# Kernel optimization log

Measured on AMD Instinct MI355X. Metric: run time of the kernel, lower is better.

## Reference

```python
import jax, jax.numpy as jnp
import numpy as np

N0, N1, N2 = 1500, 6000, 4000
F_IN, F_OUT = 32, 32
K00, K0P = 2, 2
K1N, K11, K12, K1P = 2, 2, 2, 2
K2N, K22 = 2, 2


def chebyshev(L, k, x):
    # Chebyshev recursion: T1 = L x, T2 = 2 L T1 - x, T_j = 2 L T_{j-1} - T_{j-2}
    # Returns (n, F, k) stack of T1..Tk (identity term handled by caller).
    t_prev = L @ x
    terms = [t_prev]
    t_pp = x
    for _ in range(k - 1):
        t = 2.0 * (L @ t_prev) - t_pp
        t_pp, t_prev = t_prev, t
        terms.append(t)
    return jnp.stack(terms, axis=2)


def _sym(key, n):
    a = jax.random.normal(key, (n, n), jnp.float32) / jnp.sqrt(jnp.float32(n))
    return 0.5 * (a + a.T)


def setup_inputs():
    key = jax.random.key(0)
    ks = jax.random.split(key, 16)
    x0 = jax.random.normal(ks[0], (N0, F_IN), jnp.float32)
    x1 = jax.random.normal(ks[1], (N1, F_IN), jnp.float32)
    x2 = jax.random.normal(ks[2], (N2, F_IN), jnp.float32)
    B1 = jax.random.normal(ks[3], (N0, N1), jnp.float32) / jnp.sqrt(jnp.float32(N1))
    B2 = jax.random.normal(ks[4], (N1, N2), jnp.float32) / jnp.sqrt(jnp.float32(N2))
    L0 = _sym(ks[5], N0)
    L1l = _sym(ks[6], N1)
    L1u = _sym(ks[7], N1)
    L2 = _sym(ks[8], N2)
    # Degree matrices: diagonal with strictly positive entries (as in real SC data).
    D1 = jnp.diag(jax.random.uniform(ks[9], (N0,), jnp.float32, 0.5, 2.0))
    D2 = jnp.diag(jax.random.uniform(ks[10], (N1,), jnp.float32, 0.5, 2.0))
    D3 = jnp.diag(jax.random.uniform(ks[11], (N2,), jnp.float32, 0.5, 2.0))
    D5 = jnp.diag(jax.random.uniform(ks[12], (N1,), jnp.float32, 0.5, 2.0))
    W0 = jax.random.normal(ks[13], (F_IN, F_OUT, 1 + K00 + 1 + K0P), jnp.float32) * 0.05
    W1 = jax.random.normal(ks[14], (F_IN, F_OUT, 1 + K1N + 1 + K11 + K12 + 1 + K1P), jnp.float32) * 0.05
    W2 = jax.random.normal(ks[15], (F_IN, F_OUT, 1 + K2N + 1 + K22), jnp.float32) * 0.05
    return dict(x0=x0, x1=x1, x2=x2, B1=B1, B2=B2, L0=L0, L1l=L1l, L1u=L1u,
                L2=L2, D1=D1, D2=D2, D3=D3, D5=D5, W0=W0, W1=W1, W2=W2)


def _forward(x0, x1, x2, B1, B2, L0, L1l, L1u, L2, d1_inv, d2, d3, d5_pinv, W0, W1, W2):
    # ---- order 0 ----
    x0p = d1_inv[:, None] * (B1 @ x1)               # inv(D1) @ B1 @ x1
    X0 = jnp.concatenate([x0[:, :, None], chebyshev(L0, K00, x0),
                          x0p[:, :, None], chebyshev(L0, K0P, x0p)], axis=2)
    # ---- order 1 ----
    x1n = d2[:, None] * (B1.T @ (d1_inv[:, None] * x0))  # D2 @ B1.T @ inv(D1) @ x0
    x1p = B2 @ (d3[:, None] * x2)                        # B2 @ D3 @ x2
    X1 = jnp.concatenate([x1n[:, :, None], chebyshev(L1l, K1N, x1n),
                          x1[:, :, None], chebyshev(L1l, K11, x1), chebyshev(L1u, K12, x1),
                          x1p[:, :, None], chebyshev(L1u, K1P, x1p)], axis=2)
    # ---- order 2 ----
    x2n = B2.T @ (d5_pinv[:, None] * x1)                 # B2.T @ pinv(D5) @ x1
    X2 = jnp.concatenate([x2n[:, :, None], chebyshev(L2, K2N, x2n),
                          x2[:, :, None], chebyshev(L2, K22, x2)], axis=2)
    y0 = jax.nn.relu(jnp.einsum('nik,iok->no', X0, W0))
    y1 = jax.nn.relu(jnp.einsum('nik,iok->no', X1, W1))
    y2 = jax.nn.relu(jnp.einsum('nik,iok->no', X2, W2))
    return (y0, y1, y2)


def reference(x0, x1, x2, B1, B2, L0, L1l, L1u, L2, D1, D2, D3, D5, W0, W1, W2):
    # D matrices are diagonal degree matrices; inverse/pinverse of a diagonal
    # matrix is the diagonal of (safe) reciprocals -- identical math to
    # torch.inverse / torch.pinverse on these inputs, without an O(n^3) solve.
    d1_inv = 1.0 / jnp.diag(D1)
    d2 = jnp.diag(D2)
    d3 = jnp.diag(D3)
    d5 = jnp.diag(D5)
    d5_pinv = jnp.where(d5 != 0, 1.0 / d5, 0.0)
    return _forward(x0, x1, x2, B1, B2, L0, L1l, L1u, L2, d1_inv, d2, d3, d5_pinv, W0, W1, W2)
```

## Files before the change

### kernel.cpp

```cpp
#include <hip/hip_runtime.h>
#include <stdint.h>

typedef __attribute__((ext_vector_type(4))) float f32x4;
typedef __attribute__((ext_vector_type(8))) short s16x8;
typedef unsigned short us;

static __device__ __forceinline__ us f2bf(float f) {
  union { float f; uint32_t u; } v; v.f = f;
  uint32_t u = v.u;
  u += 0x7fffu + ((u >> 16) & 1u);
  return (us)(u >> 16);
}

static __device__ __forceinline__ float dval(const float* dv, long r, long dstr, int mode) {
  if (!dv || mode == 0) return 1.f;
  float d = dv[r * dstr];
  if (mode == 2) return (d != 0.f) ? 1.f / d : 0.f;
  return d;
}

static __device__ void tpose_tile(const float* __restrict__ src, long lds_, int n,
                                  const float* __restrict__ dv, long dstr, int mode,
                                  us* __restrict__ dst, int ldn, int tile,
                                  us (*sm)[72]) {
  const int t = threadIdx.x;
  const int r0 = tile * 64;
  {
    const int rr = t & 63;
    const int cg = t >> 6;
    const int gr = r0 + rr;
    float sc = 1.f;
    f32x4 v0 = {0.f, 0.f, 0.f, 0.f}, v1 = {0.f, 0.f, 0.f, 0.f};
    if (gr < n) {
      sc = dval(dv, gr, dstr, mode);
      const float* sp = src + (long)gr * lds_ + cg * 8;
      v0 = *(const f32x4*)sp;
      v1 = *(const f32x4*)(sp + 4);
    }
#pragma unroll
    for (int j = 0; j < 4; ++j) {
      sm[cg * 8 + j][rr] = f2bf(v0[j] * sc);
      sm[cg * 8 + 4 + j][rr] = f2bf(v1[j] * sc);
    }
  }
  __syncthreads();
  {
    const int f = t >> 3;
    const int nc = (t & 7) * 8;
    if (r0 + nc < ldn) {
      s16x8 v = *(const s16x8*)&sm[f][nc];
      *(s16x8*)(dst + (size_t)f * ldn + r0 + nc) = v;
    }
  }
}

static __device__ void convT_tile(const float* __restrict__ in, int ldi, int nI, int nC,
                                  us* __restrict__ outT, int ldoT, int bx, int by,
                                  us (*sT)[72]) {
  const int t = threadIdx.x;
  const int tc0 = bx * 64;
  const int tr0 = by * 64;
  const int c0 = (t & 15) * 4;
  const int r0 = (t >> 4) * 4;
  us ub[4][4];
#pragma unroll
  for (int j = 0; j < 4; ++j) {
    int gr = tr0 + r0 + j;
    f32x4 v = {0.f, 0.f, 0.f, 0.f};
    if (gr < nI) {
      const float* pI = in + (size_t)gr * ldi + tc0 + c0;
      if (tc0 + c0 + 3 < nC) {
        v = *(const f32x4*)pI;
      } else {
#pragma unroll
        for (int jj = 0; jj < 4; ++jj) if (tc0 + c0 + jj < nC) v[jj] = pI[jj];
      }
    }
#pragma unroll
    for (int jj = 0; jj < 4; ++jj) ub[j][jj] = f2bf(v[jj]);
  }
#pragma unroll
  for (int jj = 0; jj < 4; ++jj) {
    union { us u[4]; unsigned long long ll; } w;
#pragma unroll
    for (int j = 0; j < 4; ++j) w.u[j] = ub[j][jj];
    *(unsigned long long*)&sT[c0 + jj][r0] = w.ll;
  }
  __syncthreads();
#pragma unroll
  for (int p = 0; p < 2; ++p) {
    int orow = (t >> 3) + p * 32;
    int rcol = (t & 7) * 8;
    int grow = tc0 + orow;
    int gcol = tr0 + rcol;
    if (grow < nC && gcol < ldoT) {
      union { unsigned long long ll[2]; s16x8 v; } w;
      w.ll[0] = *(const unsigned long long*)&sT[orow][rcol];
      w.ll[1] = *(const unsigned long long*)&sT[orow][rcol + 4];
      *(s16x8*)(outT + (size_t)grow * ldoT + gcol) = w.v;
    }
  }
}

struct TSeg { const float* src; us* dst; int lds_, n, ldn, start; };
struct TPack { TSeg t[8]; int nseg; };

__global__ __launch_bounds__(256) void tpose_batch(TPack P) {
  __shared__ us sm[32][72];
  int b = blockIdx.x;
  int si = P.nseg - 1;
  while (si > 0 && P.t[si].start > b) --si;
  const TSeg s = P.t[si];
  tpose_tile(s.src, s.lds_, s.n, nullptr, 0, 0, s.dst, s.ldn, b - s.start, sm);
}

__global__ __launch_bounds__(256) void prep(
    const float* __restrict__ x0, const float* __restrict__ x1, const float* __restrict__ x2,
    const float* __restrict__ D1, const float* __restrict__ D3, const float* __restrict__ D5,
    const float* __restrict__ W0, const float* __restrict__ W1, const float* __restrict__ W2,
    us* x0T, us* x0dT, us* x1T, us* x1dT, us* x2T, us* x2dT,
    us* W0T, us* W1T, us* W2T,
    float* __restrict__ X0a, float* __restrict__ X1a, float* __restrict__ X2a) {
  __shared__ us sm[32][72];
  int b = blockIdx.x;
  if (b < 24)  { tpose_tile(x0, 32, 1500, nullptr, 0, 0, x0T, 1536, b, sm); return; }
  b -= 24;
  if (b < 24)  { tpose_tile(x0, 32, 1500, D1, 1501, 2, x0dT, 1536, b, sm); return; }
  b -= 24;
  if (b < 94)  { tpose_tile(x1, 32, 6000, nullptr, 0, 0, x1T, 6016, b, sm); return; }
  b -= 94;
  if (b < 94)  { tpose_tile(x1, 32, 6000, D5, 6001, 2, x1dT, 6016, b, sm); return; }
  b -= 94;
  if (b < 63)  { tpose_tile(x2, 32, 4000, nullptr, 0, 0, x2T, 4032, b, sm); return; }
  b -= 63;
  if (b < 63)  { tpose_tile(x2, 32, 4000, D3, 4001, 1, x2dT, 4032, b, sm); return; }
  b -= 63;
  if (b < 3) {
    const float* W = (b == 0) ? W0 : ((b == 1) ? W1 : W2);
    us* dst = (b == 0) ? W0T : ((b == 1) ? W1T : W2T);
    const int K = (b == 1) ? 11 : 6;
    const int C = K * 32;
    const int CP = (b == 1) ? 384 : 192;
    for (int idx = threadIdx.x; idx < 32 * CP; idx += 256) {
      int o = idx / CP, j = idx - o * CP;
      float v = 0.f;
      if (j < C) { int k = j >> 5, i = j & 31; v = W[((long)i * 32 + o) * K + k]; }
      dst[(size_t)o * CP + j] = f2bf(v);
    }
    return;
  }
  b -= 3;
  const long V0 = 1500L * 48, V1 = 6000L * 88, V2 = 4000L * 48;
  for (long i = (long)b * 256 + threadIdx.x; i < V0 + V1 + V2; i += 512L * 256) {
    f32x4 v = {0.f, 0.f, 0.f, 0.f};
    float* dst;
    if (i < V0) {
      long r = i / 48; int c0 = (int)(i - r * 48) * 4;
      if (c0 < 32) v = *(const f32x4*)(x0 + r * 32 + c0);
      dst = X0a + r * 192 + c0;
    } else if (i < V0 + V1) {
      long j = i - V0; long r = j / 88; int c0 = (int)(j - r * 88) * 4;
      if (c0 >= 96 && c0 < 128) v = *(const f32x4*)(x1 + r * 32 + (c0 - 96));
      dst = X1a + r * 352 + c0;
    } else {
      long j = i - V0 - V1; long r = j / 48; int c0 = (int)(j - r * 48) * 4;
      if (c0 >= 96 && c0 < 128) v = *(const f32x4*)(x2 + r * 32 + (c0 - 96));
      dst = X2a + r * 192 + c0;
    }
    *(f32x4*)dst = v;
  }
}

struct Seg {
  const void* A;
  const us* Bt0; const us* Bt1;
  const float* S0; const float* S1; const float* sv;
  float* C0; float* C1;
  float alpha, beta;
  int lda, ldS, sstr, ldc;
  int n_rows, n_k, ldb, smode, kchunk, tiles, ky, start;
};
struct CSeg { const float* in; us* out; int ldi, nI, nC, ldoT, cx, start; };
struct Mega {
  Seg s[4]; CSeg c[2]; TSeg t[2];
  int nseg, gemm_end, nconv, conv_end, ntp;
};

template <int F, bool RELU, typename AT>
__global__ __launch_bounds__(256) void mega(Mega P) {
  __shared__ __align__(16) us lds[64 * 128];
  const int b = blockIdx.x;
  if (b >= P.gemm_end) {
    if (b < P.conv_end) {
      int lb = b - P.gemm_end;
      int si = P.nconv - 1;
      while (si > 0 && P.c[si].start > lb) --si;
      const CSeg s = P.c[si];
      int l = lb - s.start;
      convT_tile(s.in, s.ldi, s.nI, s.nC, s.out, s.ldoT, l % s.cx, l / s.cx, (us(*)[72])lds);
    } else {
      int lb = b - P.conv_end;
      int si = P.ntp - 1;
      while (si > 0 && P.t[si].start > lb) --si;
      const TSeg s = P.t[si];
      tpose_tile(s.src, s.lds_, s.n, nullptr, 0, 0, s.dst, s.ldn, lb - s.start, (us(*)[72])lds);
    }
    return;
  }

  us* sA = lds;
  us* sX = lds + 64 * 64;

  int si = P.nseg - 1;
  while (si > 0 && P.s[si].start > b) --si;
  const Seg sg = P.s[si];
  const int local = b - sg.start;
  const int bx = local % sg.tiles;
  const int kidx = local / sg.tiles;

  const AT* __restrict__ A = (const AT*)sg.A;
  const int n_rows = sg.n_rows, n_k = sg.n_k, ldb = sg.ldb;

  const int tid = threadIdx.x;
  const int k_begin = kidx * sg.kchunk;
  const int k_end = min(n_k, k_begin + sg.kchunk);
  const int nsteps = (k_end - k_begin + 63) >> 6;

  const int srow = tid >> 2;
  const int sslot = tid & 3;
  const int kc_off = sslot * 16;
  const long arowg = (long)bx * 64 + srow;
  const bool arow_ok = arowg < n_rows;
  const bool xrow_ok = (F == 64) || (srow < 32);
  const us* xbase = ((srow < 32) ? sg.Bt0 : sg.Bt1) + (size_t)(srow & 31) * ldb;

  s16x8 abf0 = (s16x8)0, abf1 = (s16x8)0;
  f32x4 af0, af1, af2, af3;
  s16x8 x0r = (s16x8)0, x1r = (s16x8)0;

  auto load_tiles = [&](int k0) {
    int kc = k0 + kc_off;
    if constexpr (sizeof(AT) == 4) {
      af0 = f32x4{0, 0, 0, 0}; af1 = af0; af2 = af0; af3 = af0;
      if (arow_ok) {
        const float* ap = (const float*)A + (size_t)arowg * sg.lda + kc;
        if (kc + 15 < n_k) {
          af0 = *(const f32x4*)ap; af1 = *(const f32x4*)(ap + 4);
          af2 = *(const f32x4*)(ap + 8); af3 = *(const f32x4*)(ap + 12);
        } else {
#pragma unroll
          for (int j = 0; j < 4; ++j) {
            if (kc + j < n_k) af0[j] = ap[j];
            if (kc + 4 + j < n_k) af1[j] = ap[4 + j];
            if (kc + 8 + j < n_k) af2[j] = ap[8 + j];
            if (kc + 12 + j < n_k) af3[j] = ap[12 + j];
          }
        }
      }
    } else {
      abf0 = (s16x8)0; abf1 = (s16x8)0;
      if (arow_ok) {
        const us* ap = (const us*)A + (size_t)arowg * sg.lda + kc;
        if (kc + 15 < n_k) {
          abf0 = *(const s16x8*)ap; abf1 = *(const s16x8*)(ap + 8);
        } else {
#pragma unroll
          for (int j = 0; j < 8; ++j) {
            if (kc + j < n_k) abf0[j] = (short)ap[j];
            if (kc + 8 + j < n_k) abf1[j] = (short)ap[8 + j];
          }
        }
      }
    }
    if (xrow_ok) {
      x0r = *(const s16x8*)(xbase + kc);
      x1r = *(const s16x8*)(xbase + kc + 8);
    }
  };

  load_tiles(k_begin);

  const int wave = tid >> 6;
  const int lane = tid & 63;
  const int g = lane >> 4;
  const int r = lane & 15;
  const int wslot0 = ((2 * sslot) ^ (srow & 7)) * 8;
  const int wslot1 = ((2 * sslot + 1) ^ (srow & 7)) * 8;

  f32x4 acc[F / 16];
#pragma unroll
  for (int i = 0; i < F / 16; ++i) acc[i] = f32x4{0.f, 0.f, 0.f, 0.f};

  for (int s = 0; s < nsteps; ++s) {
    s16x8 pk0, pk1;
    if constexpr (sizeof(AT) == 4) {
#pragma unroll
      for (int j = 0; j < 4; ++j) {
        pk0[j] = (short)f2bf(af0[j]); pk0[4 + j] = (short)f2bf(af1[j]);
        pk1[j] = (short)f2bf(af2[j]); pk1[4 + j] = (short)f2bf(af3[j]);
      }
    } else { pk0 = abf0; pk1 = abf1; }
    *(s16x8*)&sA[srow * 64 + wslot0] = pk0;
    *(s16x8*)&sA[srow * 64 + wslot1] = pk1;
    if (xrow_ok) {
      *(s16x8*)&sX[srow * 64 + wslot0] = x0r;
      *(s16x8*)&sX[srow * 64 + wslot1] = x1r;
    }
    __syncthreads();
    if (s + 1 < nsteps) load_tiles(k_begin + (s + 1) * 64);

    const int arow = wave * 16 + r;
#pragma unroll
    for (int kk = 0; kk < 2; ++kk) {
      s16x8 afr = *(s16x8*)&sA[arow * 64 + (((kk * 4 + g) ^ (arow & 7)) << 3)];
#pragma unroll
      for (int nt = 0; nt < F / 16; ++nt) {
        int xc = nt * 16 + r;
        s16x8 bfr = *(s16x8*)&sX[xc * 64 + (((kk * 4 + g) ^ (xc & 7)) << 3)];
        acc[nt] = __builtin_amdgcn_mfma_f32_16x16x32_bf16(afr, bfr, acc[nt], 0, 0, 0);
      }
    }
    __syncthreads();
  }

  float svv[4];
#pragma unroll
  for (int j = 0; j < 4; ++j) {
    long row = (long)bx * 64 + wave * 16 + g * 4 + j;
    svv[j] = (row < n_rows) ? dval(sg.sv, row, sg.sstr, sg.smode) : 0.f;
  }
#pragma unroll
  for (int nt = 0; nt < F / 16; ++nt) {
    float* C = (F == 64 && nt >= 2) ? sg.C1 : sg.C0;
    const float* S = (F == 64 && nt >= 2) ? sg.S1 : sg.S0;
    int col = ((F == 64) ? (nt & 1) : nt) * 16 + r;
#pragma unroll
    for (int j = 0; j < 4; ++j) {
      long row = (long)bx * 64 + wave * 16 + g * 4 + j;
      if (row < n_rows) {
        float v = sg.alpha * acc[nt][j] * svv[j];
        if (S && (sg.ky == 1 || kidx == 0)) v += sg.beta * S[row * (size_t)sg.ldS + col];
        if (sg.ky > 1) {
          atomicAdd(&C[row * (size_t)sg.ldc + col], v);
        } else {
          if (RELU) v = fmaxf(v, 0.0f);
          C[row * (size_t)sg.ldc + col] = v;
        }
      }
    }
  }
}

__global__ void colcopy(float* __restrict__ dst, const float* __restrict__ src, int n,
                        const float* __restrict__ dv, long dstr, int mode) {
  int idx = blockIdx.x * 256 + threadIdx.x;
  if (idx >= n * 32) return;
  dst[idx] = src[idx] * dval(dv, idx >> 5, dstr, mode);
}
__global__ void scale_ld(float* __restrict__ dst, long ld, int n,
                         const float* __restrict__ dv, long dstr, int mode) {
  int idx = blockIdx.x * 256 + threadIdx.x;
  if (idx >= n * 32) return;
  dst[(size_t)(idx >> 5) * ld + (idx & 31)] *= dval(dv, idx >> 5, dstr, mode);
}
__global__ __launch_bounds__(256) void mm_at(
    const float* __restrict__ A, int lda, int m,
    const float* __restrict__ X,
    float* __restrict__ C, int ldc, int n, int kchunk) {
  const int fg = threadIdx.x & 3;
  const int cg = threadIdx.x >> 2;
  const int c = blockIdx.x * 256 + cg * 4;
  const int k0 = blockIdx.y * kchunk;
  const int k1 = min(m, k0 + kchunk);
  const int f = fg * 8;
  float acc[4][8];
#pragma unroll
  for (int a = 0; a < 4; ++a)
#pragma unroll
    for (int bb = 0; bb < 8; ++bb) acc[a][bb] = 0.f;
  for (int k = k0; k < k1; ++k) {
    const float* Ar = A + (size_t)k * lda + c;
    f32x4 a;
    if (c + 3 < n) a = *(const f32x4*)Ar;
    else {
      a = f32x4{0.f, 0.f, 0.f, 0.f};
#pragma unroll
      for (int j = 0; j < 4; ++j) if (c + j < n) a[j] = Ar[j];
    }
    f32x4 xa = *(const f32x4*)(X + (size_t)k * 32 + f);
    f32x4 xb = *(const f32x4*)(X + (size_t)k * 32 + f + 4);
#pragma unroll
    for (int cc = 0; cc < 4; ++cc)
#pragma unroll
      for (int jj = 0; jj < 4; ++jj) {
        acc[cc][jj] += a[cc] * xa[jj];
        acc[cc][4 + jj] += a[cc] * xb[jj];
      }
  }
  if (c >= n) return;
#pragma unroll
  for (int cc = 0; cc < 4; ++cc) {
    if (c + cc >= n) break;
#pragma unroll
    for (int jj = 0; jj < 8; ++jj)
      atomicAdd(&C[(size_t)(c + cc) * ldc + f + jj], acc[cc][jj]);
  }
}


extern "C" void kernel_launch(void* const* d_in, const int* in_sizes, int n_in,
                              void* d_out, int out_size, void* d_ws, size_t ws_size,
                              hipStream_t stream) {
  (void)in_sizes; (void)n_in; (void)out_size;
  const float* x0  = (const float*)d_in[0];
  const float* x1  = (const float*)d_in[1];
  const float* x2  = (const float*)d_in[2];
  const float* B1  = (const float*)d_in[3];
  const float* B2  = (const float*)d_in[4];
  const float* L0  = (const float*)d_in[5];
  const float* L1l = (const float*)d_in[6];
  const float* L1u = (const float*)d_in[7];
  const float* L2  = (const float*)d_in[8];
  const float* D1  = (const float*)d_in[9];
  const float* D2  = (const float*)d_in[10];
  const float* D3  = (const float*)d_in[11];
  const float* D5  = (const float*)d_in[12];
  const float* W0  = (const float*)d_in[13];
  const float* W1  = (const float*)d_in[14];
  const float* W2  = (const float*)d_in[15];
  float* out = (float*)d_out;

  char* p = (char*)d_ws;
  auto alloc = [&](size_t b) { char* r = p; p += (b + 255) & ~(size_t)255; return r; };

  us* x0T   = (us*)alloc((size_t)32 * 1536 * 2);
  us* x0dT  = (us*)alloc((size_t)32 * 1536 * 2);
  us* x1T   = (us*)alloc((size_t)32 * 6016 * 2);
  us* x1dT  = (us*)alloc((size_t)32 * 6016 * 2);
  us* x2T   = (us*)alloc((size_t)32 * 4032 * 2);
  us* x2dT  = (us*)alloc((size_t)32 * 4032 * 2);
  us* x0pT  = (us*)alloc((size_t)32 * 1536 * 2);
  us* x1nT  = (us*)alloc((size_t)32 * 6016 * 2);
  us* x1pT  = (us*)alloc((size_t)32 * 6016 * 2);
  us* x2nT  = (us*)alloc((size_t)32 * 4032 * 2);
  us* T1a0T = (us*)alloc((size_t)32 * 1536 * 2);
  us* T1b0T = (us*)alloc((size_t)32 * 1536 * 2);
  us* T1laT = (us*)alloc((size_t)32 * 6016 * 2);
  us* T1lbT = (us*)alloc((size_t)32 * 6016 * 2);
  us* T1uaT = (us*)alloc((size_t)32 * 6016 * 2);
  us* T1ubT = (us*)alloc((size_t)32 * 6016 * 2);
  us* T1a2T = (us*)alloc((size_t)32 * 4032 * 2);
  us* T1b2T = (us*)alloc((size_t)32 * 4032 * 2);
  us* W0T   = (us*)alloc((size_t)32 * 192 * 2);
  us* W1T   = (us*)alloc((size_t)32 * 384 * 2);
  us* W2T   = (us*)alloc((size_t)32 * 192 * 2);

  float* X0a = (float*)alloc((size_t)1500 * 192 * 4);
  float* X1a = (float*)alloc((size_t)6000 * 352 * 4);
  float* X2a = (float*)alloc((size_t)4000 * 192 * 4);

  float* z0  = (float*)alloc((size_t)1500 * 32 * 4);
  float* sx1 = (float*)alloc((size_t)6000 * 32 * 4);

  size_t used = (size_t)(p - (char*)d_ws);
  const size_t needB = (size_t)6000 * 1536 * 2 + (size_t)4000 * 6016 * 2 + 1024;
  bool haveB = used + needB <= ws_size;
  us *B1t = nullptr, *B2t = nullptr;
  if (haveB) {
    B1t = (us*)alloc((size_t)6000 * 1536 * 2);
    B2t = (us*)alloc((size_t)4000 * 6016 * 2);
  }

  auto nb = [](long t) { return (unsigned)((t + 255) / 256); };
  auto seg = [](const void* A, int lda, int n_rows, int n_k,
                const us* Bt0, const us* Bt1, int ldb,
                float alpha, const float* S0, const float* S1, int ldS, float beta,
                const float* sv, int sstr, int smode,
                float* C0, float* C1, int ldc,
                int kchunk, int tiles, int ky, int start) {
    Seg s;
    s.A = A; s.Bt0 = Bt0; s.Bt1 = Bt1; s.S0 = S0; s.S1 = S1; s.sv = sv;
    s.C0 = C0; s.C1 = C1; s.alpha = alpha; s.beta = beta;
    s.lda = lda; s.ldS = ldS; s.sstr = sstr; s.ldc = ldc;
    s.n_rows = n_rows; s.n_k = n_k; s.ldb = ldb; s.smode = smode;
    s.kchunk = kchunk; s.tiles = tiles; s.ky = ky; s.start = start;
    return s;
  };

  prep<<<877, 256, 0, stream>>>(x0, x1, x2, D1, D3, D5, W0, W1, W2,
                                x0T, x0dT, x1T, x1dT, x2T, x2dT, W0T, W1T, W2T,
                                X0a, X1a, X2a);

  {
    Mega P{};
    P.nseg = 2;
    P.s[0] = seg(B1, 6000, 1500, 6000, x1T, x1T, 6016,
                 1.f, nullptr, nullptr, 0, 0.f, D1, 1501, 2,
                 X0a + 3 * 32, nullptr, 192, 768, 24, 8, 0);
    P.s[1] = seg(B2, 4000, 6000, 4000, x2dT, x2dT, 4032,
                 1.f, nullptr, nullptr, 0, 0.f, nullptr, 0, 0,
                 X1a + 8 * 32, nullptr, 352, 512, 94, 8, 192);
    P.gemm_end = 944;
    if (haveB) {
      P.nconv = 2;
      P.c[0] = CSeg{B1, B1t, 6000, 1500, 6000, 1536, 94, 0};
      P.c[1] = CSeg{B2, B2t, 4000, 6000, 4000, 6016, 63, 2256};
      P.conv_end = 944 + 8178;
    } else {
      P.nconv = 0; P.conv_end = 944;
    }
    P.ntp = 0;
    mega<32, false, float><<<P.conv_end, 256, 0, stream>>>(P);
  }

  if (haveB) {
    Mega P{};
    P.nseg = 2;
    P.s[0] = seg(B1t, 1536, 6000, 1536, x0dT, x0dT, 1536,
                 1.f, nullptr, nullptr, 0, 0.f, D2, 6001, 1,
                 X1a + 0 * 32, nullptr, 352, 384, 94, 4, 0);
    P.s[1] = seg(B2t, 6016, 4000, 6016, x1dT, x1dT, 6016,
                 1.f, nullptr, nullptr, 0, 0.f, nullptr, 0, 0,
                 X2a + 0 * 32, nullptr, 192, 768, 63, 8, 376);
    P.gemm_end = 880;
    P.nconv = 0; P.conv_end = 880;
    P.ntp = 2;
    P.t[0] = TSeg{X0a + 3 * 32, x0pT, 192, 1500, 1536, 0};
    P.t[1] = TSeg{X1a + 8 * 32, x1pT, 352, 6000, 6016, 24};
    mega<32, false, us><<<998, 256, 0, stream>>>(P);
  } else {
    colcopy<<<nb(1500L * 32), 256, 0, stream>>>(z0, x0, 1500, D1, 1501, 2);
    mm_at<<<dim3(24, 24), 256, 0, stream>>>(B1, 6000, 1500, z0, X1a + 0 * 32, 352, 6000, 63);
    scale_ld<<<nb(6000L * 32), 256, 0, stream>>>(X1a + 0 * 32, 352, 6000, D2, 6001, 1);
    colcopy<<<nb(6000L * 32), 256, 0, stream>>>(sx1, x1, 6000, D5, 6001, 2);
    mm_at<<<dim3(16, 32), 256, 0, stream>>>(B2, 4000, 6000, sx1, X2a + 0 * 32, 192, 4000, 188);
    TPack T{};
    T.nseg = 2;
    T.t[0] = TSeg{X0a + 3 * 32, x0pT, 192, 1500, 1536, 0};
    T.t[1] = TSeg{X1a + 8 * 32, x1pT, 352, 6000, 6016, 24};
    tpose_batch<<<118, 256, 0, stream>>>(T);
  }

  {
    TPack T{};
    T.nseg = 2;
    T.t[0] = TSeg{X1a + 0 * 32, x1nT, 352, 6000, 6016, 0};
    T.t[1] = TSeg{X2a + 0 * 32, x2nT, 192, 4000, 4032, 94};
    tpose_batch<<<157, 256, 0, stream>>>(T);
  }

  {
    Mega P{};
    P.nseg = 4;
    P.s[0] = seg(L0, 1500, 1500, 1500, x0T, x0pT, 1536,
                 1.f, nullptr, nullptr, 0, 0.f, nullptr, 0, 0,
                 X0a + 1 * 32, X0a + 4 * 32, 192, 768, 24, 2, 0);
    P.s[1] = seg(L1l, 6000, 6000, 6000, x1nT, x1T, 6016,
                 1.f, nullptr, nullptr, 0, 0.f, nullptr, 0, 0,
                 X1a + 1 * 32, X1a + 4 * 32, 352, 1536, 94, 4, 48);
    P.s[2] = seg(L1u, 6000, 6000, 6000, x1T, x1pT, 6016,
                 1.f, nullptr, nullptr, 0, 0.f, nullptr, 0, 0,
                 X1a + 6 * 32, X1a + 9 * 32, 352, 1536, 94, 4, 424);
    P.s[3] = seg(L2, 4000, 4000, 4000, x2nT, x2T, 4032,
                 1.f, nullptr, nullptr, 0, 0.f, nullptr, 0, 0,
                 X2a + 1 * 32, X2a + 4 * 32, 192, 1024, 63, 4, 800);
    P.gemm_end = 1052; P.nconv = 0; P.conv_end = 1052; P.ntp = 0;
    mega<64, false, float><<<1052, 256, 0, stream>>>(P);
  }

  {
    TPack T{};
    T.nseg = 8;
    T.t[0] = TSeg{X0a + 1 * 32, T1a0T, 192, 1500, 1536, 0};
    T.t[1] = TSeg{X0a + 4 * 32, T1b0T, 192, 1500, 1536, 24};
    T.t[2] = TSeg{X1a + 1 * 32, T1laT, 352, 6000, 6016, 48};
    T.t[3] = TSeg{X1a + 4 * 32, T1lbT, 352, 6000, 6016, 142};
    T.t[4] = TSeg{X1a + 6 * 32, T1uaT, 352, 6000, 6016, 236};
    T.t[5] = TSeg{X1a + 9 * 32, T1ubT, 352, 6000, 6016, 330};
    T.t[6] = TSeg{X2a + 1 * 32, T1a2T, 192, 4000, 4032, 424};
    T.t[7] = TSeg{X2a + 4 * 32, T1b2T, 192, 4000, 4032, 487};
    tpose_batch<<<550, 256, 0, stream>>>(T);
  }

  {
    Mega P{};
    P.nseg = 4;
    P.s[0] = seg(L0, 1500, 1500, 1500, T1a0T, T1b0T, 1536,
                 2.f, X0a + 0 * 32, X0a + 3 * 32, 192, -1.f, nullptr, 0, 0,
                 X0a + 2 * 32, X0a + 5 * 32, 192, 768, 24, 2, 0);
    P.s[1] = seg(L1l, 6000, 6000, 6000, T1laT, T1lbT, 6016,
                 2.f, X1a + 0 * 32, X1a + 3 * 32, 352, -1.f, nullptr, 0, 0,
                 X1a + 2 * 32, X1a + 5 * 32, 352, 1536, 94, 4, 48);
    P.s[2] = seg(L1u, 6000, 6000, 6000, T1uaT, T1ubT, 6016,
                 2.f, X1a + 3 * 32, X1a + 8 * 32, 352, -1.f, nullptr, 0, 0,
                 X1a + 7 * 32, X1a + 10 * 32, 352, 1536, 94, 4, 424);
    P.s[3] = seg(L2, 4000, 4000, 4000, T1a2T, T1b2T, 4032,
                 2.f, X2a + 0 * 32, X2a + 3 * 32, 192, -1.f, nullptr, 0, 0,
                 X2a + 2 * 32, X2a + 5 * 32, 192, 1024, 63, 4, 800);
    P.gemm_end = 1052; P.nconv = 0; P.conv_end = 1052; P.ntp = 0;
    mega<64, false, float><<<1052, 256, 0, stream>>>(P);
  }

  {
    Mega P{};
    P.nseg = 3;
    P.s[0] = seg(X0a, 192, 1500, 192, W0T, W0T, 192,
                 1.f, nullptr, nullptr, 0, 0.f, nullptr, 0, 0,
                 out, nullptr, 32, 192, 24, 1, 0);
    P.s[1] = seg(X1a, 352, 6000, 352, W1T, W1T, 384,
                 1.f, nullptr, nullptr, 0, 0.f, nullptr, 0, 0,
                 out + 48000, nullptr, 32, 384, 94, 1, 24);
    P.s[2] = seg(X2a, 192, 4000, 192, W2T, W2T, 192,
                 1.f, nullptr, nullptr, 0, 0.f, nullptr, 0, 0,
                 out + 240000, nullptr, 32, 192, 63, 1, 118);
    P.gemm_end = 181; P.nconv = 0; P.conv_end = 181; P.ntp = 0;
    mega<32, true, float><<<181, 256, 0, stream>>>(P);
  }
}
```

Measured before the change: 308.0 us.

## Double-buffer LDS tiles and prefetch two K-steps ahead in GEMM loop

Splits the shared-memory staging into two ping-pong buffers and keeps two register sets of prefetched global tiles, so loads run two K-steps ahead. This drops the trailing __syncthreads per step, leaving one barrier per step, and replaces the leading one with an explicit lgkmcnt wait plus s_barrier fenced by sched_barriers. It raises LDS use to 32 KB and the register pressure, which can lower occupancy.

```diff
diff --git a/kernel.cpp b/kernel.cpp
--- a/kernel.cpp
+++ b/kernel.cpp
@@ -188,7 +188,7 @@
 
 template <int F, bool RELU, typename AT>
 __global__ __launch_bounds__(256) void mega(Mega P) {
-  __shared__ __align__(16) us lds[64 * 128];
+  __shared__ __align__(16) us lds[4 * 64 * 64];
   const int b = blockIdx.x;
   if (b >= P.gemm_end) {
     if (b < P.conv_end) {
@@ -208,9 +208,6 @@
     return;
   }
 
-  us* sA = lds;
-  us* sX = lds + 64 * 64;
-
   int si = P.nseg - 1;
   while (si > 0 && P.s[si].start > b) --si;
   const Seg sg = P.s[si];
@@ -234,51 +231,50 @@
   const bool xrow_ok = (F == 64) || (srow < 32);
   const us* xbase = ((srow < 32) ? sg.Bt0 : sg.Bt1) + (size_t)(srow & 31) * ldb;
 
-  s16x8 abf0 = (s16x8)0, abf1 = (s16x8)0;
-  f32x4 af0, af1, af2, af3;
-  s16x8 x0r = (s16x8)0, x1r = (s16x8)0;
-
-  auto load_tiles = [&](int k0) {
+  f32x4 aA0, aA1, aA2, aA3, aB0, aB1, aB2, aB3;
+  s16x8 bA0 = (s16x8)0, bA1 = (s16x8)0, bB0 = (s16x8)0, bB1 = (s16x8)0;
+  s16x8 xA0 = (s16x8)0, xA1 = (s16x8)0, xB0 = (s16x8)0, xB1 = (s16x8)0;
+
+  auto load_set = [&](int k0, f32x4& a0, f32x4& a1, f32x4& a2, f32x4& a3,
+                      s16x8& b0, s16x8& b1, s16x8& xx0, s16x8& xx1) {
     int kc = k0 + kc_off;
     if constexpr (sizeof(AT) == 4) {
-      af0 = f32x4{0, 0, 0, 0}; af1 = af0; af2 = af0; af3 = af0;
+      a0 = f32x4{0, 0, 0, 0}; a1 = a0; a2 = a0; a3 = a0;
       if (arow_ok) {
         const float* ap = (const float*)A + (size_t)arowg * sg.lda + kc;
         if (kc + 15 < n_k) {
-          af0 = *(const f32x4*)ap; af1 = *(const f32x4*)(ap + 4);
-          af2 = *(const f32x4*)(ap + 8); af3 = *(const f32x4*)(ap + 12);
+          a0 = *(const f32x4*)ap; a1 = *(const f32x4*)(ap + 4);
+          a2 = *(const f32x4*)(ap + 8); a3 = *(const f32x4*)(ap + 12);
         } else {
 #pragma unroll
           for (int j = 0; j < 4; ++j) {
-            if (kc + j < n_k) af0[j] = ap[j];
-            if (kc + 4 + j < n_k) af1[j] = ap[4 + j];
-            if (kc + 8 + j < n_k) af2[j] = ap[8 + j];
-            if (kc + 12 + j < n_k) af3[j] = ap[12 + j];
+            if (kc + j < n_k) a0[j] = ap[j];
+            if (kc + 4 + j < n_k) a1[j] = ap[4 + j];
+            if (kc + 8 + j < n_k) a2[j] = ap[8 + j];
+            if (kc + 12 + j < n_k) a3[j] = ap[12 + j];
           }
         }
       }
     } else {
-      abf0 = (s16x8)0; abf1 = (s16x8)0;
+      b0 = (s16x8)0; b1 = (s16x8)0;
       if (arow_ok) {
         const us* ap = (const us*)A + (size_t)arowg * sg.lda + kc;
         if (kc + 15 < n_k) {
-          abf0 = *(const s16x8*)ap; abf1 = *(const s16x8*)(ap + 8);
+          b0 = *(const s16x8*)ap; b1 = *(const s16x8*)(ap + 8);
         } else {
 #pragma unroll
           for (int j = 0; j < 8; ++j) {
-            if (kc + j < n_k) abf0[j] = (short)ap[j];
-            if (kc + 8 + j < n_k) abf1[j] = (short)ap[8 + j];
+            if (kc + j < n_k) b0[j] = (short)ap[j];
+            if (kc + 8 + j < n_k) b1[j] = (short)ap[8 + j];
           }
         }
       }
     }
     if (xrow_ok) {
-      x0r = *(const s16x8*)(xbase + kc);
-      x1r = *(const s16x8*)(xbase + kc + 8);
+      xx0 = *(const s16x8*)(xbase + kc);
+      xx1 = *(const s16x8*)(xbase + kc + 8);
     }
   };
-
-  load_tiles(k_begin);
 
   const int wave = tid >> 6;
   const int lane = tid & 63;
@@ -291,24 +287,29 @@
 #pragma unroll
   for (int i = 0; i < F / 16; ++i) acc[i] = f32x4{0.f, 0.f, 0.f, 0.f};
 
-  for (int s = 0; s < nsteps; ++s) {
+  auto step = [&](int s, int bufsel, f32x4& a0, f32x4& a1, f32x4& a2, f32x4& a3,
+                  s16x8& b0, s16x8& b1, s16x8& xx0, s16x8& xx1) {
+    us* sA = lds + (bufsel ? 8192 : 0);
+    us* sX = sA + 4096;
     s16x8 pk0, pk1;
     if constexpr (sizeof(AT) == 4) {
 #pragma unroll
       for (int j = 0; j < 4; ++j) {
-        pk0[j] = (short)f2bf(af0[j]); pk0[4 + j] = (short)f2bf(af1[j]);
-        pk1[j] = (short)f2bf(af2[j]); pk1[4 + j] = (short)f2bf(af3[j]);
+        pk0[j] = (short)f2bf(a0[j]); pk0[4 + j] = (short)f2bf(a1[j]);
+        pk1[j] = (short)f2bf(a2[j]); pk1[4 + j] = (short)f2bf(a3[j]);
       }
-    } else { pk0 = abf0; pk1 = abf1; }
+    } else { pk0 = b0; pk1 = b1; }
     *(s16x8*)&sA[srow * 64 + wslot0] = pk0;
     *(s16x8*)&sA[srow * 64 + wslot1] = pk1;
     if (xrow_ok) {
-      *(s16x8*)&sX[srow * 64 + wslot0] = x0r;
-      *(s16x8*)&sX[srow * 64 + wslot1] = x1r;
-    }
-    __syncthreads();
-    if (s + 1 < nsteps) load_tiles(k_begin + (s + 1) * 64);
-
+      *(s16x8*)&sX[srow * 64 + wslot0] = xx0;
+      *(s16x8*)&sX[srow * 64 + wslot1] = xx1;
+    }
+    __builtin_amdgcn_sched_barrier(0);
+    asm volatile("s_waitcnt lgkmcnt(0)" ::: "memory");
+    __builtin_amdgcn_s_barrier();
+    __builtin_amdgcn_sched_barrier(0);
+    if (s + 2 < nsteps) load_set(k_begin + (s + 2) * 64, a0, a1, a2, a3, b0, b1, xx0, xx1);
     const int arow = wave * 16 + r;
 #pragma unroll
     for (int kk = 0; kk < 2; ++kk) {
@@ -320,7 +321,13 @@
         acc[nt] = __builtin_amdgcn_mfma_f32_16x16x32_bf16(afr, bfr, acc[nt], 0, 0, 0);
       }
     }
-    __syncthreads();
+  };
+
+  load_set(k_begin, aA0, aA1, aA2, aA3, bA0, bA1, xA0, xA1);
+  if (nsteps > 1) load_set(k_begin + 64, aB0, aB1, aB2, aB3, bB0, bB1, xB0, xB1);
+  for (int s = 0; s < nsteps; s += 2) {
+    step(s, 0, aA0, aA1, aA2, aA3, bA0, bA1, xA0, xA1);
+    if (s + 1 < nsteps) step(s + 1, 1, aB0, aB1, aB2, aB3, bB0, bB1, xB0, xB1);
   }
 
   float svv[4];
```

New measurement: 313.4 us. About the same (+1.8%).

## Double GEMM row tile to 128 rows per block and rebalance K-splits

Applied to the files above, without the earlier changes.

The mega GEMM kernel now computes 128 rows per block: each wave handles two 16-row subtiles that share the same X fragments loaded from LDS, and each thread loads 32 A elements per step. Launch configurations are updated to halve the tile counts, and for the L1/L2 Chebyshev GEMMs the K-split is raised to keep the grid size similar. This is meant to reuse the staged X tile across twice as many A rows, cutting X global and LDS traffic. The cost is more LDS and registers per block, which can lower occupancy, and fewer blocks for the small GEMMs such as the final weight projection.

```diff
diff --git a/kernel.cpp b/kernel.cpp
--- a/kernel.cpp
+++ b/kernel.cpp
@@ -188,7 +188,7 @@
 
 template <int F, bool RELU, typename AT>
 __global__ __launch_bounds__(256) void mega(Mega P) {
-  __shared__ __align__(16) us lds[64 * 128];
+  __shared__ __align__(16) us lds[128 * 64 + 64 * 64];
   const int b = blockIdx.x;
   if (b >= P.gemm_end) {
     if (b < P.conv_end) {
@@ -209,7 +209,7 @@
   }
 
   us* sA = lds;
-  us* sX = lds + 64 * 64;
+  us* sX = lds + 128 * 64;
 
   int si = P.nseg - 1;
   while (si > 0 && P.s[si].start > b) --si;
@@ -226,55 +226,59 @@
   const int k_end = min(n_k, k_begin + sg.kchunk);
   const int nsteps = (k_end - k_begin + 63) >> 6;
 
-  const int srow = tid >> 2;
-  const int sslot = tid & 3;
-  const int kc_off = sslot * 16;
-  const long arowg = (long)bx * 64 + srow;
+  const int srowA = tid >> 1;
+  const int sslotA = tid & 1;
+  const int kcA = sslotA * 32;
+  const long arowg = (long)bx * 128 + srowA;
   const bool arow_ok = arowg < n_rows;
-  const bool xrow_ok = (F == 64) || (srow < 32);
-  const us* xbase = ((srow < 32) ? sg.Bt0 : sg.Bt1) + (size_t)(srow & 31) * ldb;
-
-  s16x8 abf0 = (s16x8)0, abf1 = (s16x8)0;
-  f32x4 af0, af1, af2, af3;
+  const int srowX = tid >> 2;
+  const int sslotX = tid & 3;
+  const int kcX = sslotX * 16;
+  const bool xrow_ok = (F == 64) || (srowX < 32);
+  const us* xbase = ((srowX < 32) ? sg.Bt0 : sg.Bt1) + (size_t)(srowX & 31) * ldb;
+
+  f32x4 af[8];
+  s16x8 abf[4];
   s16x8 x0r = (s16x8)0, x1r = (s16x8)0;
 
   auto load_tiles = [&](int k0) {
-    int kc = k0 + kc_off;
+    int kc = k0 + kcA;
     if constexpr (sizeof(AT) == 4) {
-      af0 = f32x4{0, 0, 0, 0}; af1 = af0; af2 = af0; af3 = af0;
+#pragma unroll
+      for (int h = 0; h < 8; ++h) af[h] = f32x4{0.f, 0.f, 0.f, 0.f};
       if (arow_ok) {
         const float* ap = (const float*)A + (size_t)arowg * sg.lda + kc;
-        if (kc + 15 < n_k) {
-          af0 = *(const f32x4*)ap; af1 = *(const f32x4*)(ap + 4);
-          af2 = *(const f32x4*)(ap + 8); af3 = *(const f32x4*)(ap + 12);
+        if (kc + 31 < n_k) {
+#pragma unroll
+          for (int h = 0; h < 8; ++h) af[h] = *(const f32x4*)(ap + 4 * h);
         } else {
 #pragma unroll
-          for (int j = 0; j < 4; ++j) {
-            if (kc + j < n_k) af0[j] = ap[j];
-            if (kc + 4 + j < n_k) af1[j] = ap[4 + j];
-            if (kc + 8 + j < n_k) af2[j] = ap[8 + j];
-            if (kc + 12 + j < n_k) af3[j] = ap[12 + j];
-          }
+          for (int h = 0; h < 8; ++h)
+#pragma unroll
+            for (int j = 0; j < 4; ++j)
+              if (kc + 4 * h + j < n_k) af[h][j] = ap[4 * h + j];
         }
       }
     } else {
-      abf0 = (s16x8)0; abf1 = (s16x8)0;
+#pragma unroll
+      for (int h = 0; h < 4; ++h) abf[h] = (s16x8)0;
       if (arow_ok) {
         const us* ap = (const us*)A + (size_t)arowg * sg.lda + kc;
-        if (kc + 15 < n_k) {
-          abf0 = *(const s16x8*)ap; abf1 = *(const s16x8*)(ap + 8);
+        if (kc + 31 < n_k) {
+#pragma unroll
+          for (int h = 0; h < 4; ++h) abf[h] = *(const s16x8*)(ap + 8 * h);
         } else {
 #pragma unroll
-          for (int j = 0; j < 8; ++j) {
-            if (kc + j < n_k) abf0[j] = (short)ap[j];
-            if (kc + 8 + j < n_k) abf1[j] = (short)ap[8 + j];
-          }
+          for (int h = 0; h < 4; ++h)
+#pragma unroll
+            for (int j = 0; j < 8; ++j)
+              if (kc + 8 * h + j < n_k) abf[h][j] = (short)ap[8 * h + j];
         }
       }
     }
     if (xrow_ok) {
-      x0r = *(const s16x8*)(xbase + kc);
-      x1r = *(const s16x8*)(xbase + kc + 8);
+      x0r = *(const s16x8*)(xbase + k0 + kcX);
+      x1r = *(const s16x8*)(xbase + k0 + kcX + 8);
     }
   };
 
@@ -284,67 +288,80 @@
   const int lane = tid & 63;
   const int g = lane >> 4;
   const int r = lane & 15;
-  const int wslot0 = ((2 * sslot) ^ (srow & 7)) * 8;
-  const int wslot1 = ((2 * sslot + 1) ^ (srow & 7)) * 8;
-
-  f32x4 acc[F / 16];
-#pragma unroll
-  for (int i = 0; i < F / 16; ++i) acc[i] = f32x4{0.f, 0.f, 0.f, 0.f};
+  const int wsX0 = ((2 * sslotX) ^ (srowX & 7)) * 8;
+  const int wsX1 = ((2 * sslotX + 1) ^ (srowX & 7)) * 8;
+
+  f32x4 acc[2][F / 16];
+#pragma unroll
+  for (int st = 0; st < 2; ++st)
+#pragma unroll
+    for (int i = 0; i < F / 16; ++i) acc[st][i] = f32x4{0.f, 0.f, 0.f, 0.f};
 
   for (int s = 0; s < nsteps; ++s) {
-    s16x8 pk0, pk1;
-    if constexpr (sizeof(AT) == 4) {
-#pragma unroll
-      for (int j = 0; j < 4; ++j) {
-        pk0[j] = (short)f2bf(af0[j]); pk0[4 + j] = (short)f2bf(af1[j]);
-        pk1[j] = (short)f2bf(af2[j]); pk1[4 + j] = (short)f2bf(af3[j]);
+#pragma unroll
+    for (int h = 0; h < 4; ++h) {
+      s16x8 pk;
+      if constexpr (sizeof(AT) == 4) {
+#pragma unroll
+        for (int j = 0; j < 4; ++j) {
+          pk[j] = (short)f2bf(af[2 * h][j]);
+          pk[4 + j] = (short)f2bf(af[2 * h + 1][j]);
+        }
+      } else {
+        pk = abf[h];
       }
-    } else { pk0 = abf0; pk1 = abf1; }
-    *(s16x8*)&sA[srow * 64 + wslot0] = pk0;
-    *(s16x8*)&sA[srow * 64 + wslot1] = pk1;
+      const int ws = ((4 * sslotA + h) ^ (srowA & 7)) * 8;
+      *(s16x8*)&sA[srowA * 64 + ws] = pk;
+    }
     if (xrow_ok) {
-      *(s16x8*)&sX[srow * 64 + wslot0] = x0r;
-      *(s16x8*)&sX[srow * 64 + wslot1] = x1r;
+      *(s16x8*)&sX[srowX * 64 + wsX0] = x0r;
+      *(s16x8*)&sX[srowX * 64 + wsX1] = x1r;
     }
     __syncthreads();
     if (s + 1 < nsteps) load_tiles(k_begin + (s + 1) * 64);
 
-    const int arow = wave * 16 + r;
-#pragma unroll
-    for (int kk = 0; kk < 2; ++kk) {
-      s16x8 afr = *(s16x8*)&sA[arow * 64 + (((kk * 4 + g) ^ (arow & 7)) << 3)];
-#pragma unroll
-      for (int nt = 0; nt < F / 16; ++nt) {
-        int xc = nt * 16 + r;
-        s16x8 bfr = *(s16x8*)&sX[xc * 64 + (((kk * 4 + g) ^ (xc & 7)) << 3)];
-        acc[nt] = __builtin_amdgcn_mfma_f32_16x16x32_bf16(afr, bfr, acc[nt], 0, 0, 0);
+#pragma unroll
+    for (int st = 0; st < 2; ++st) {
+      const int arow = wave * 32 + st * 16 + r;
+#pragma unroll
+      for (int kk = 0; kk < 2; ++kk) {
+        s16x8 afr = *(s16x8*)&sA[arow * 64 + (((kk * 4 + g) ^ (arow & 7)) << 3)];
+#pragma unroll
+        for (int nt = 0; nt < F / 16; ++nt) {
+          int xc = nt * 16 + r;
+          s16x8 bfr = *(s16x8*)&sX[xc * 64 + (((kk * 4 + g) ^ (xc & 7)) << 3)];
+          acc[st][nt] = __builtin_amdgcn_mfma_f32_16x16x32_bf16(afr, bfr, acc[st][nt], 0, 0, 0);
+        }
       }
     }
     __syncthreads();
   }
 
-  float svv[4];
-#pragma unroll
-  for (int j = 0; j < 4; ++j) {
-    long row = (long)bx * 64 + wave * 16 + g * 4 + j;
-    svv[j] = (row < n_rows) ? dval(sg.sv, row, sg.sstr, sg.smode) : 0.f;
-  }
-#pragma unroll
-  for (int nt = 0; nt < F / 16; ++nt) {
-    float* C = (F == 64 && nt >= 2) ? sg.C1 : sg.C0;
-    const float* S = (F == 64 && nt >= 2) ? sg.S1 : sg.S0;
-    int col = ((F == 64) ? (nt & 1) : nt) * 16 + r;
+#pragma unroll
+  for (int st = 0; st < 2; ++st) {
+    float svv[4];
 #pragma unroll
     for (int j = 0; j < 4; ++j) {
-      long row = (long)bx * 64 + wave * 16 + g * 4 + j;
-      if (row < n_rows) {
-        float v = sg.alpha * acc[nt][j] * svv[j];
-        if (S && (sg.ky == 1 || kidx == 0)) v += sg.beta * S[row * (size_t)sg.ldS + col];
-        if (sg.ky > 1) {
-          atomicAdd(&C[row * (size_t)sg.ldc + col], v);
-        } else {
-          if (RELU) v = fmaxf(v, 0.0f);
-          C[row * (size_t)sg.ldc + col] = v;
+      long row = (long)bx * 128 + wave * 32 + st * 16 + g * 4 + j;
+      svv[j] = (row < n_rows) ? dval(sg.sv, row, sg.sstr, sg.smode) : 0.f;
+    }
+#pragma unroll
+    for (int nt = 0; nt < F / 16; ++nt) {
+      float* C = (F == 64 && nt >= 2) ? sg.C1 : sg.C0;
+      const float* S = (F == 64 && nt >= 2) ? sg.S1 : sg.S0;
+      int col = ((F == 64) ? (nt & 1) : nt) * 16 + r;
+#pragma unroll
+      for (int j = 0; j < 4; ++j) {
+        long row = (long)bx * 128 + wave * 32 + st * 16 + g * 4 + j;
+        if (row < n_rows) {
+          float v = sg.alpha * acc[st][nt][j] * svv[j];
+          if (S && (sg.ky == 1 || kidx == 0)) v += sg.beta * S[row * (size_t)sg.ldS + col];
+          if (sg.ky > 1) {
+            atomicAdd(&C[row * (size_t)sg.ldc + col], v);
+          } else {
+            if (RELU) v = fmaxf(v, 0.0f);
+            C[row * (size_t)sg.ldc + col] = v;
+          }
         }
       }
     }
@@ -496,18 +513,18 @@
     P.nseg = 2;
     P.s[0] = seg(B1, 6000, 1500, 6000, x1T, x1T, 6016,
                  1.f, nullptr, nullptr, 0, 0.f, D1, 1501, 2,
-                 X0a + 3 * 32, nullptr, 192, 768, 24, 8, 0);
+                 X0a + 3 * 32, nullptr, 192, 768, 12, 8, 0);
     P.s[1] = seg(B2, 4000, 6000, 4000, x2dT, x2dT, 4032,
                  1.f, nullptr, nullptr, 0, 0.f, nullptr, 0, 0,
-                 X1a + 8 * 32, nullptr, 352, 512, 94, 8, 192);
-    P.gemm_end = 944;
+                 X1a + 8 * 32, nullptr, 352, 512, 47, 8, 96);
+    P.gemm_end = 472;
     if (haveB) {
       P.nconv = 2;
       P.c[0] = CSeg{B1, B1t, 6000, 1500, 6000, 1536, 94, 0};
       P.c[1] = CSeg{B2, B2t, 4000, 6000, 4000, 6016, 63, 2256};
-      P.conv_end = 944 + 8178;
+      P.conv_end = 472 + 8178;
     } else {
-      P.nconv = 0; P.conv_end = 944;
+      P.nconv = 0; P.conv_end = 472;
     }
     P.ntp = 0;
     mega<32, false, float><<<P.conv_end, 256, 0, stream>>>(P);
@@ -518,16 +535,16 @@
     P.nseg = 2;
     P.s[0] = seg(B1t, 1536, 6000, 1536, x0dT, x0dT, 1536,
                  1.f, nullptr, nullptr, 0, 0.f, D2, 6001, 1,
-                 X1a + 0 * 32, nullptr, 352, 384, 94, 4, 0);
+                 X1a + 0 * 32, nullptr, 352, 384, 47, 4, 0);
     P.s[1] = seg(B2t, 6016, 4000, 6016, x1dT, x1dT, 6016,
                  1.f, nullptr, nullptr, 0, 0.f, nullptr, 0, 0,
-                 X2a + 0 * 32, nullptr, 192, 768, 63, 8, 376);
-    P.gemm_end = 880;
-    P.nconv = 0; P.conv_end = 880;
+                 X2a + 0 * 32, nullptr, 192, 768, 32, 8, 188);
+    P.gemm_end = 444;
+    P.nconv = 0; P.conv_end = 444;
     P.ntp = 2;
     P.t[0] = TSeg{X0a + 3 * 32, x0pT, 192, 1500, 1536, 0};
     P.t[1] = TSeg{X1a + 8 * 32, x1pT, 352, 6000, 6016, 24};
-    mega<32, false, us><<<998, 256, 0, stream>>>(P);
+    mega<32, false, us><<<562, 256, 0, stream>>>(P);
   } else {
     colcopy<<<nb(1500L * 32), 256, 0, stream>>>(z0, x0, 1500, D1, 1501, 2);
     mm_at<<<dim3(24, 24), 256, 0, stream>>>(B1, 6000, 1500, z0, X1a + 0 * 32, 352, 6000, 63);
@@ -554,18 +571,18 @@
     P.nseg = 4;
     P.s[0] = seg(L0, 1500, 1500, 1500, x0T, x0pT, 1536,
                  1.f, nullptr, nullptr, 0, 0.f, nullptr, 0, 0,
-                 X0a + 1 * 32, X0a + 4 * 32, 192, 768, 24, 2, 0);
+                 X0a + 1 * 32, X0a + 4 * 32, 192, 768, 12, 2, 0);
     P.s[1] = seg(L1l, 6000, 6000, 6000, x1nT, x1T, 6016,
                  1.f, nullptr, nullptr, 0, 0.f, nullptr, 0, 0,
-                 X1a + 1 * 32, X1a + 4 * 32, 352, 1536, 94, 4, 48);
+                 X1a + 1 * 32, X1a + 4 * 32, 352, 768, 47, 8, 24);
     P.s[2] = seg(L1u, 6000, 6000, 6000, x1T, x1pT, 6016,
                  1.f, nullptr, nullptr, 0, 0.f, nullptr, 0, 0,
-                 X1a + 6 * 32, X1a + 9 * 32, 352, 1536, 94, 4, 424);
+                 X1a + 6 * 32, X1a + 9 * 32, 352, 768, 47, 8, 400);
     P.s[3] = seg(L2, 4000, 4000, 4000, x2nT, x2T, 4032,
                  1.f, nullptr, nullptr, 0, 0.f, nullptr, 0, 0,
-                 X2a + 1 * 32, X2a + 4 * 32, 192, 1024, 63, 4, 800);
-    P.gemm_end = 1052; P.nconv = 0; P.conv_end = 1052; P.ntp = 0;
-    mega<64, false, float><<<1052, 256, 0, stream>>>(P);
+                 X2a + 1 * 32, X2a + 4 * 32, 192, 512, 32, 8, 776);
+    P.gemm_end = 1032; P.nconv = 0; P.conv_end = 1032; P.ntp = 0;
+    mega<64, false, float><<<1032, 256, 0, stream>>>(P);
   }
 
   {
@@ -587,18 +604,18 @@
     P.nseg = 4;
     P.s[0] = seg(L0, 1500, 1500, 1500, T1a0T, T1b0T, 1536,
                  2.f, X0a + 0 * 32, X0a + 3 * 32, 192, -1.f, nullptr, 0, 0,
-                 X0a + 2 * 32, X0a + 5 * 32, 192, 768, 24, 2, 0);
+                 X0a + 2 * 32, X0a + 5 * 32, 192, 768, 12, 2, 0);
     P.s[1] = seg(L1l, 6000, 6000, 6000, T1laT, T1lbT, 6016,
                  2.f, X1a + 0 * 32, X1a + 3 * 32, 352, -1.f, nullptr, 0, 0,
-                 X1a + 2 * 32, X1a + 5 * 32, 352, 1536, 94, 4, 48);
+                 X1a + 2 * 32, X1a + 5 * 32, 352, 768, 47, 8, 24);
     P.s[2] = seg(L1u, 6000, 6000, 6000, T1uaT, T1ubT, 6016,
                  2.f, X1a + 3 * 32, X1a + 8 * 32, 352, -1.f, nullptr, 0, 0,
-                 X1a + 7 * 32, X1a + 10 * 32, 352, 1536, 94, 4, 424);
+                 X1a + 7 * 32, X1a + 10 * 32, 352, 768, 47, 8, 400);
     P.s[3] = seg(L2, 4000, 4000, 4000, T1a2T, T1b2T, 4032,
                  2.f, X2a + 0 * 32, X2a + 3 * 32, 192, -1.f, nullptr, 0, 0,
-                 X2a + 2 * 32, X2a + 5 * 32, 192, 1024, 63, 4, 800);
-    P.gemm_end = 1052; P.nconv = 0; P.conv_end = 1052; P.ntp = 0;
-    mega<64, false, float><<<1052, 256, 0, stream>>>(P);
+                 X2a + 2 * 32, X2a + 5 * 32, 192, 512, 32, 8, 776);
+    P.gemm_end = 1032; P.nconv = 0; P.conv_end = 1032; P.ntp = 0;
+    mega<64, false, float><<<1032, 256, 0, stream>>>(P);
   }
 
   {
@@ -606,14 +623,14 @@
     P.nseg = 3;
     P.s[0] = seg(X0a, 192, 1500, 192, W0T, W0T, 192,
                  1.f, nullptr, nullptr, 0, 0.f, nullptr, 0, 0,
-                 out, nullptr, 32, 192, 24, 1, 0);
+                 out, nullptr, 32, 192, 12, 1, 0);
     P.s[1] = seg(X1a, 352, 6000, 352, W1T, W1T, 384,
                  1.f, nullptr, nullptr, 0, 0.f, nullptr, 0, 0,
-                 out + 48000, nullptr, 32, 384, 94, 1, 24);
+                 out + 48000, nullptr, 32, 384, 47, 1, 12);
     P.s[2] = seg(X2a, 192, 4000, 192, W2T, W2T, 192,
                  1.f, nullptr, nullptr, 0, 0.f, nullptr, 0, 0,
-                 out + 240000, nullptr, 32, 192, 63, 1, 118);
-    P.gemm_end = 181; P.nconv = 0; P.conv_end = 181; P.ntp = 0;
-    mega<32, true, float><<<181, 256, 0, stream>>>(P);
-  }
-}
+                 out + 240000, nullptr, 32, 192, 32, 1, 59);
+    P.gemm_end = 91; P.nconv = 0; P.conv_end = 91; P.ntp = 0;
+    mega<32, true, float><<<91, 256, 0, stream>>>(P);
+  }
+}
```

Result: slower. 360.8 us (+17.1%).
